# Performance work log

Measured on AMD Instinct MI355X. Metric: run time of the kernel, lower is better.

Reference implementation:

```python
import jax, jax.numpy as jnp
import numpy as np

BETA = 0.2
GAMMA = 0.95
N_NODES = 100000
N_EDGES = 1600000
D = 64


def setup_inputs() -> dict:
    key = jax.random.key(0)
    k1, k2, k3, k4 = jax.random.split(key, 4)
    z = jax.random.normal(k1, (N_NODES, D), dtype=jnp.float32)
    e = jax.random.uniform(k2, (N_EDGES, 2, D), dtype=jnp.float32)
    src = jax.random.randint(k3, (N_EDGES,), 0, N_NODES, dtype=jnp.int64)
    dst = jax.random.randint(k4, (N_EDGES,), 0, N_NODES, dtype=jnp.int64)
    return {"z": z, "e": e, "src": src, "dst": dst}


def reference(z, e, src, dst):
    # DGL update_all with message_func/reduce_func from GATLayer.bp:
    #   q  = GAMMA * max(z[src], axis=-1, keepdims=True) * e[:,1,:] + e[:,0,:]
    #   ac = e[:,1,:]
    #   z' = BETA*z + (1-BETA) * sum_q / (sum_ac + 1e-6)   (only for nodes with in-edges)
    n = z.shape[0]
    zmax = jnp.max(z, axis=-1, keepdims=True)  # [N, 1]
    e0 = e[:, 0, :]                            # [E, D]
    e1 = e[:, 1, :]                            # [E, D]
    q = GAMMA * zmax[src] * e1 + e0            # edge gather + elementwise
    sum_q = jax.ops.segment_sum(q, dst, num_segments=n)    # scatter-sum reduce
    sum_ac = jax.ops.segment_sum(e1, dst, num_segments=n)
    z_new = BETA * z + (1.0 - BETA) * sum_q / (sum_ac + 1e-6)
    # DGL only runs reduce_func on nodes that received messages; others keep z.
    deg = jax.ops.segment_sum(jnp.ones(dst.shape, dtype=z.dtype), dst, num_segments=n)
    return jnp.where(deg[:, None] > 0, z_new, z)
```

## Files before the change

### kernel.cpp

```cpp
#include <hip/hip_runtime.h>

#define DD 64
constexpr float BETA  = 0.2f;
constexpr float GAMMA = 0.95f;

typedef float f4 __attribute__((ext_vector_type(4)));

__global__ void zmax_kernel(const float* __restrict__ z, float* __restrict__ zmax,
                            int* __restrict__ counts, int n) {
    int wid  = blockIdx.x * (blockDim.x >> 6) + (threadIdx.x >> 6);
    int lane = threadIdx.x & 63;
    int r = lane >> 4;
    int c = lane & 15;
    int node = wid * 4 + r;
    if (node >= n) return;
    f4 v = ((const f4*)(z + (long)node * DD))[c];
    float m = fmaxf(fmaxf(v.x, v.y), fmaxf(v.z, v.w));
    #pragma unroll
    for (int off = 1; off < 16; off <<= 1)
        m = fmaxf(m, __shfl_xor(m, off, 64));
    if (c == 0) { zmax[node] = m; counts[node] = 0; }
}

__global__ void hist_kernel(const int* __restrict__ dst, int* __restrict__ counts, int nE) {
    int i = (blockIdx.x * blockDim.x + threadIdx.x) * 4;
    if (i + 3 < nE) {
        int4 d = *(const int4*)(dst + i);
        atomicAdd(&counts[d.x], 1); atomicAdd(&counts[d.y], 1);
        atomicAdd(&counts[d.z], 1); atomicAdd(&counts[d.w], 1);
    } else {
        for (int j = i; j < nE; j++) atomicAdd(&counts[dst[j]], 1);
    }
}

__global__ void scan_local_kernel(const int* __restrict__ counts, int* __restrict__ base,
                                  int* __restrict__ bsums, int n) {
    __shared__ int warp_sums[4];
    int t = threadIdx.x;
    int lane = t & 63, w = t >> 6;
    int g0 = blockIdx.x * 1024 + t * 4;
    int c[4];
    int s = 0;
    #pragma unroll
    for (int j = 0; j < 4; j++) {
        c[j] = (g0 + j < n) ? counts[g0 + j] : 0;
        s += c[j];
    }
    int v = s;
    #pragma unroll
    for (int off = 1; off < 64; off <<= 1) {
        int u = __shfl_up(v, off, 64);
        if (lane >= off) v += u;
    }
    if (lane == 63) warp_sums[w] = v;
    __syncthreads();
    int wo = 0;
    for (int k = 0; k < w; k++) wo += warp_sums[k];
    int acc = wo + v - s;
    #pragma unroll
    for (int j = 0; j < 4; j++) {
        if (g0 + j < n) base[g0 + j] = acc;
        acc += c[j];
    }
    if (t == 255) bsums[blockIdx.x] = wo + v;
}

__global__ void scan_bsums_kernel(int* __restrict__ bsums, int nb) {
    __shared__ int warp_sums[4];
    int t = threadIdx.x, lane = t & 63, w = t >> 6;
    int s = (t < nb) ? bsums[t] : 0;
    int v = s;
    #pragma unroll
    for (int off = 1; off < 64; off <<= 1) {
        int u = __shfl_up(v, off, 64);
        if (lane >= off) v += u;
    }
    if (lane == 63) warp_sums[w] = v;
    __syncthreads();
    int wo = 0;
    for (int k = 0; k < w; k++) wo += warp_sums[k];
    if (t < nb) bsums[t] = wo + v - s;
}

__global__ void add_off_kernel(int* __restrict__ base, int* __restrict__ cursor,
                               const int* __restrict__ bsums, int n) {
    int i = blockIdx.x * blockDim.x + threadIdx.x;
    if (i >= n) return;
    int b = base[i] + bsums[i >> 10];
    base[i] = b;
    cursor[i] = b;
}

__global__ void scatter_kernel(const int* __restrict__ dst, int* __restrict__ cursor,
                               int* __restrict__ perm, int nE) {
    int i = (blockIdx.x * blockDim.x + threadIdx.x) * 4;
    if (i + 3 < nE) {
        int4 d = *(const int4*)(dst + i);
        perm[atomicAdd(&cursor[d.x], 1)] = i;
        perm[atomicAdd(&cursor[d.y], 1)] = i + 1;
        perm[atomicAdd(&cursor[d.z], 1)] = i + 2;
        perm[atomicAdd(&cursor[d.w], 1)] = i + 3;
    } else {
        for (int j = i; j < nE; j++) perm[atomicAdd(&cursor[dst[j]], 1)] = j;
    }
}

__global__ void gather_kernel(const float* __restrict__ z,
                              const float* __restrict__ e,
                              const int* __restrict__ src,
                              const float* __restrict__ zmax,
                              const int* __restrict__ base,
                              const int* __restrict__ counts,
                              const int* __restrict__ perm,
                              float* __restrict__ out, int n) {
    int node = blockIdx.x * (blockDim.x >> 6) + (threadIdx.x >> 6);
    int lane = threadIdx.x & 63;
    if (node >= n) return;
    int c = lane & 31;
    int p = lane >> 5;

    f4 zi = ((const f4*)(z + (long)node * DD))[lane & 15];

    int degv = counts[node];
    if (degv == 0) {
        if (lane < 16) ((f4*)(out + (long)node * DD))[lane] = zi;
        return;
    }
    int start = base[node];

    float a1x = 0, a1y = 0, a1z = 0, a1w = 0;
    float a2x = 0, a2y = 0, a2z = 0, a2w = 0;

    int done = 0;
    while (done < degv) {
        int batch = min(degv - done, 64);
        int eidv = 0; float zmv = 0.0f;
        if (lane < batch) {
            eidv = __builtin_nontemporal_load(perm + start + done + lane);
            zmv  = GAMMA * zmax[src[eidv]];
        }
        int npair = (batch + 1) >> 1;
        int t = 0;
        for (; t + 4 <= npair; t += 4) {
            int k0 = 2 * t + p, k1 = k0 + 2, k2 = k0 + 4, k3 = k0 + 6;
            int eid0 = __shfl(eidv, k0, 64);
            int eid1 = __shfl(eidv, k1, 64);
            int eid2 = __shfl(eidv, k2, 64);
            int eid3 = __shfl(eidv, k3, 64);
            f4 v0 = __builtin_nontemporal_load((const f4*)(e + (long)eid0 * (2 * DD)) + c);
            f4 v1 = __builtin_nontemporal_load((const f4*)(e + (long)eid1 * (2 * DD)) + c);
            f4 v2 = __builtin_nontemporal_load((const f4*)(e + (long)eid2 * (2 * DD)) + c);
            f4 v3 = __builtin_nontemporal_load((const f4*)(e + (long)eid3 * (2 * DD)) + c);
            float zm0 = __shfl(zmv, k0, 64);
            float zm1 = __shfl(zmv, k1, 64);
            float zm2 = __shfl(zmv, k2, 64);
            float zm3 = __shfl(zmv, k3, 64);
            float w0 = (k0 < batch) ? 1.0f : 0.0f;
            float w1 = (k1 < batch) ? 1.0f : 0.0f;
            float w2 = (k2 < batch) ? 1.0f : 0.0f;
            float w3 = (k3 < batch) ? 1.0f : 0.0f;
            a1x = fmaf(w0, v0.x, a1x); a1y = fmaf(w0, v0.y, a1y);
            a1z = fmaf(w0, v0.z, a1z); a1w = fmaf(w0, v0.w, a1w);
            a2x = fmaf(zm0, v0.x, a2x); a2y = fmaf(zm0, v0.y, a2y);
            a2z = fmaf(zm0, v0.z, a2z); a2w = fmaf(zm0, v0.w, a2w);
            a1x = fmaf(w1, v1.x, a1x); a1y = fmaf(w1, v1.y, a1y);
            a1z = fmaf(w1, v1.z, a1z); a1w = fmaf(w1, v1.w, a1w);
            a2x = fmaf(zm1, v1.x, a2x); a2y = fmaf(zm1, v1.y, a2y);
            a2z = fmaf(zm1, v1.z, a2z); a2w = fmaf(zm1, v1.w, a2w);
            a1x = fmaf(w2, v2.x, a1x); a1y = fmaf(w2, v2.y, a1y);
            a1z = fmaf(w2, v2.z, a1z); a1w = fmaf(w2, v2.w, a1w);
            a2x = fmaf(zm2, v2.x, a2x); a2y = fmaf(zm2, v2.y, a2y);
            a2z = fmaf(zm2, v2.z, a2z); a2w = fmaf(zm2, v2.w, a2w);
            a1x = fmaf(w3, v3.x, a1x); a1y = fmaf(w3, v3.y, a1y);
            a1z = fmaf(w3, v3.z, a1z); a1w = fmaf(w3, v3.w, a1w);
            a2x = fmaf(zm3, v3.x, a2x); a2y = fmaf(zm3, v3.y, a2y);
            a2z = fmaf(zm3, v3.z, a2z); a2w = fmaf(zm3, v3.w, a2w);
        }
        for (; t < npair; t++) {
            int k = 2 * t + p;
            int   eid = __shfl(eidv, k, 64);
            float zm  = __shfl(zmv, k, 64);
            float w   = (k < batch) ? 1.0f : 0.0f;
            f4 v = __builtin_nontemporal_load((const f4*)(e + (long)eid * (2 * DD)) + c);
            a1x = fmaf(w, v.x, a1x); a1y = fmaf(w, v.y, a1y);
            a1z = fmaf(w, v.z, a1z); a1w = fmaf(w, v.w, a1w);
            a2x = fmaf(zm, v.x, a2x); a2y = fmaf(zm, v.y, a2y);
            a2z = fmaf(zm, v.z, a2z); a2w = fmaf(zm, v.w, a2w);
        }
        done += batch;
    }

    a1x += __shfl_xor(a1x, 32, 64); a1y += __shfl_xor(a1y, 32, 64);
    a1z += __shfl_xor(a1z, 32, 64); a1w += __shfl_xor(a1w, 32, 64);
    a2x += __shfl_xor(a2x, 32, 64); a2y += __shfl_xor(a2y, 32, 64);
    a2z += __shfl_xor(a2z, 32, 64); a2w += __shfl_xor(a2w, 32, 64);

    int pl = (lane & 15) + 16;
    float sax = __shfl(a1x, pl, 64), say = __shfl(a1y, pl, 64);
    float saz = __shfl(a1z, pl, 64), saw = __shfl(a1w, pl, 64);
    float sqx = a1x + __shfl(a2x, pl, 64);
    float sqy = a1y + __shfl(a2y, pl, 64);
    float sqz = a1z + __shfl(a2z, pl, 64);
    float sqw = a1w + __shfl(a2w, pl, 64);

    if (lane < 16) {
        const float ob = 1.0f - BETA;
        f4 r;
        r.x = fmaf(BETA, zi.x, ob * sqx / (sax + 1e-6f));
        r.y = fmaf(BETA, zi.y, ob * sqy / (say + 1e-6f));
        r.z = fmaf(BETA, zi.z, ob * sqz / (saz + 1e-6f));
        r.w = fmaf(BETA, zi.w, ob * sqw / (saw + 1e-6f));
        ((f4*)(out + (long)node * DD))[lane] = r;
    }
}

extern "C" void kernel_launch(void* const* d_in, const int* in_sizes, int n_in,
                              void* d_out, int out_size, void* d_ws, size_t ws_size,
                              hipStream_t stream) {
    const float* z   = (const float*)d_in[0];
    const float* e   = (const float*)d_in[1];
    const int*   src = (const int*)d_in[2];
    const int*   dst = (const int*)d_in[3];
    float* out = (float*)d_out;

    int n  = in_sizes[0] / DD;
    int nE = in_sizes[2];
    int nb = (n + 1023) / 1024;

    char* ws = (char*)d_ws;
    size_t off = 0;
    auto alloc = [&](size_t bytes) { void* q = ws + off; off = (off + bytes + 255) & ~255ull; return q; };
    float* zmax  = (float*)alloc((size_t)n * 4);
    int* counts  = (int*)alloc((size_t)n * 4);
    int* base    = (int*)alloc((size_t)n * 4);
    int* cursor  = (int*)alloc((size_t)n * 4);
    int* bsums   = (int*)alloc((size_t)nb * 4);
    int* perm    = (int*)alloc((size_t)nE * 4);

    zmax_kernel<<<(n + 15) / 16, 256, 0, stream>>>(z, zmax, counts, n);
    hist_kernel<<<(nE / 4 + 255) / 256, 256, 0, stream>>>(dst, counts, nE);
    scan_local_kernel<<<nb, 256, 0, stream>>>(counts, base, bsums, n);
    scan_bsums_kernel<<<1, 256, 0, stream>>>(bsums, nb);
    add_off_kernel<<<(n + 255) / 256, 256, 0, stream>>>(base, cursor, bsums, n);
    scatter_kernel<<<(nE / 4 + 255) / 256, 256, 0, stream>>>(dst, cursor, perm, nE);
    gather_kernel<<<(n + 3) / 4, 256, 0, stream>>>(z, e, src, zmax, base, counts, perm, out, n);
}
```

Measured before the change: 360.0 us.

## Precompute per-edge gamma*zmax[src] and scatter it into CSR order

Per-edge GAMMA*zmax[src] is now computed in the histogram pass with coalesced src reads and stored per edge. The scatter pass writes it into CSR order next to perm, so the gather kernel reads it contiguously. This removes the dependent random src[eid] then zmax[...] chain from the gather's critical path. In exchange it adds two edge-sized float buffers plus extra random writes in the scatter and extra reads in the histogram pass.

```diff
diff --git a/kernel.cpp b/kernel.cpp
--- a/kernel.cpp
+++ b/kernel.cpp
@@ -22,14 +22,24 @@
     if (c == 0) { zmax[node] = m; counts[node] = 0; }
 }
 
-__global__ void hist_kernel(const int* __restrict__ dst, int* __restrict__ counts, int nE) {
+__global__ void hist_zmq_kernel(const int* __restrict__ dst, const int* __restrict__ src,
+                                const float* __restrict__ zmax,
+                                int* __restrict__ counts, float* __restrict__ zmq, int nE) {
     int i = (blockIdx.x * blockDim.x + threadIdx.x) * 4;
     if (i + 3 < nE) {
         int4 d = *(const int4*)(dst + i);
         atomicAdd(&counts[d.x], 1); atomicAdd(&counts[d.y], 1);
         atomicAdd(&counts[d.z], 1); atomicAdd(&counts[d.w], 1);
+        int4 s = *(const int4*)(src + i);
+        f4 q;
+        q.x = GAMMA * zmax[s.x]; q.y = GAMMA * zmax[s.y];
+        q.z = GAMMA * zmax[s.z]; q.w = GAMMA * zmax[s.w];
+        *(f4*)(zmq + i) = q;
     } else {
-        for (int j = i; j < nE; j++) atomicAdd(&counts[dst[j]], 1);
+        for (int j = i; j < nE; j++) {
+            atomicAdd(&counts[dst[j]], 1);
+            zmq[j] = GAMMA * zmax[src[j]];
+        }
     }
 }
 
@@ -91,27 +101,35 @@
     cursor[i] = b;
 }
 
-__global__ void scatter_kernel(const int* __restrict__ dst, int* __restrict__ cursor,
-                               int* __restrict__ perm, int nE) {
+__global__ void scatter_kernel(const int* __restrict__ dst, const float* __restrict__ zmq,
+                               int* __restrict__ cursor,
+                               int* __restrict__ perm, float* __restrict__ zmq_csr, int nE) {
     int i = (blockIdx.x * blockDim.x + threadIdx.x) * 4;
     if (i + 3 < nE) {
         int4 d = *(const int4*)(dst + i);
-        perm[atomicAdd(&cursor[d.x], 1)] = i;
-        perm[atomicAdd(&cursor[d.y], 1)] = i + 1;
-        perm[atomicAdd(&cursor[d.z], 1)] = i + 2;
-        perm[atomicAdd(&cursor[d.w], 1)] = i + 3;
+        f4 q = *(const f4*)(zmq + i);
+        int p0 = atomicAdd(&cursor[d.x], 1);
+        int p1 = atomicAdd(&cursor[d.y], 1);
+        int p2 = atomicAdd(&cursor[d.z], 1);
+        int p3 = atomicAdd(&cursor[d.w], 1);
+        perm[p0] = i;     zmq_csr[p0] = q.x;
+        perm[p1] = i + 1; zmq_csr[p1] = q.y;
+        perm[p2] = i + 2; zmq_csr[p2] = q.z;
+        perm[p3] = i + 3; zmq_csr[p3] = q.w;
     } else {
-        for (int j = i; j < nE; j++) perm[atomicAdd(&cursor[dst[j]], 1)] = j;
+        for (int j = i; j < nE; j++) {
+            int p = atomicAdd(&cursor[dst[j]], 1);
+            perm[p] = j; zmq_csr[p] = zmq[j];
+        }
     }
 }
 
 __global__ void gather_kernel(const float* __restrict__ z,
                               const float* __restrict__ e,
-                              const int* __restrict__ src,
-                              const float* __restrict__ zmax,
                               const int* __restrict__ base,
                               const int* __restrict__ counts,
                               const int* __restrict__ perm,
+                              const float* __restrict__ zmq_csr,
                               float* __restrict__ out, int n) {
     int node = blockIdx.x * (blockDim.x >> 6) + (threadIdx.x >> 6);
     int lane = threadIdx.x & 63;
@@ -137,7 +155,7 @@
         int eidv = 0; float zmv = 0.0f;
         if (lane < batch) {
             eidv = __builtin_nontemporal_load(perm + start + done + lane);
-            zmv  = GAMMA * zmax[src[eidv]];
+            zmv  = __builtin_nontemporal_load(zmq_csr + start + done + lane);
         }
         int npair = (batch + 1) >> 1;
         int t = 0;
@@ -230,18 +248,20 @@
     char* ws = (char*)d_ws;
     size_t off = 0;
     auto alloc = [&](size_t bytes) { void* q = ws + off; off = (off + bytes + 255) & ~255ull; return q; };
-    float* zmax  = (float*)alloc((size_t)n * 4);
-    int* counts  = (int*)alloc((size_t)n * 4);
-    int* base    = (int*)alloc((size_t)n * 4);
-    int* cursor  = (int*)alloc((size_t)n * 4);
-    int* bsums   = (int*)alloc((size_t)nb * 4);
-    int* perm    = (int*)alloc((size_t)nE * 4);
+    float* zmax    = (float*)alloc((size_t)n * 4);
+    int* counts    = (int*)alloc((size_t)n * 4);
+    int* base      = (int*)alloc((size_t)n * 4);
+    int* cursor    = (int*)alloc((size_t)n * 4);
+    int* bsums     = (int*)alloc((size_t)nb * 4);
+    int* perm      = (int*)alloc((size_t)nE * 4);
+    float* zmq     = (float*)alloc((size_t)nE * 4);
+    float* zmq_csr = (float*)alloc((size_t)nE * 4);
 
     zmax_kernel<<<(n + 15) / 16, 256, 0, stream>>>(z, zmax, counts, n);
-    hist_kernel<<<(nE / 4 + 255) / 256, 256, 0, stream>>>(dst, counts, nE);
+    hist_zmq_kernel<<<(nE / 4 + 255) / 256, 256, 0, stream>>>(dst, src, zmax, counts, zmq, nE);
     scan_local_kernel<<<nb, 256, 0, stream>>>(counts, base, bsums, n);
     scan_bsums_kernel<<<1, 256, 0, stream>>>(bsums, nb);
     add_off_kernel<<<(n + 255) / 256, 256, 0, stream>>>(base, cursor, bsums, n);
-    scatter_kernel<<<(nE / 4 + 255) / 256, 256, 0, stream>>>(dst, cursor, perm, nE);
-    gather_kernel<<<(n + 3) / 4, 256, 0, stream>>>(z, e, src, zmax, base, counts, perm, out, n);
-}
+    scatter_kernel<<<(nE / 4 + 255) / 256, 256, 0, stream>>>(dst, zmq, cursor, perm, zmq_csr, nE);
+    gather_kernel<<<(n + 3) / 4, 256, 0, stream>>>(z, e, base, counts, perm, zmq_csr, out, n);
+}
```

New measurement: 348.8 us. 3.1% less time.
